# Kernel tuning notes

Measured on AMD Instinct MI355X. Metric: run time of the kernel, lower is better.

The kernel has to match this reference:

```python
import jax, jax.numpy as jnp
import numpy as np

PLANES, RATIO = 512, 4
Q = PLANES // RATIO  # 128
B, H, W = 4, 128, 128


def _dw_stride2(x, k):
    # depthwise 3x3 stride-2 conv, NCHW, kernel [C,1,3,3]
    return jax.lax.conv_general_dilated(
        x, k, window_strides=(2, 2), padding=((1, 1), (1, 1)),
        feature_group_count=x.shape[1],
        dimension_numbers=('NCHW', 'OIHW', 'NCHW'))


def _upsample_bilinear_ac(x, out_h, out_w):
    # bilinear, align_corners=True (matches F.interpolate)
    n, c, h, w = x.shape
    def co(out, ins):
        s = (ins - 1) / (out - 1)
        pos = jnp.arange(out, dtype=jnp.float32) * jnp.float32(s)
        i0 = jnp.floor(pos).astype(jnp.int32)
        i1 = jnp.minimum(i0 + 1, ins - 1)
        return i0, i1, pos - i0.astype(jnp.float32)
    y0, y1, ty = co(out_h, h)
    x0, x1, tx = co(out_w, w)
    rows = x[:, :, y0, :] * (1 - ty)[None, None, :, None] + x[:, :, y1, :] * ty[None, None, :, None]
    return rows[:, :, :, x0] * (1 - tx) + rows[:, :, :, x1] * tx


def setup_inputs() -> dict:
    key = jax.random.key(0)
    ks = jax.random.split(key, 32)
    nrm = lambda k, s, sc=0.05: jax.random.normal(k, s, jnp.float32) * sc
    uni = lambda k, s: jax.random.uniform(k, s, jnp.float32, 0.5, 1.5)
    return {
        'feat': jax.random.normal(ks[0], (B, PLANES, H, W), jnp.float32),
        'w_phi': nrm(ks[1], (2 * Q, PLANES)),
        'bn_phi_s': uni(ks[2], (2 * Q,)), 'bn_phi_b': nrm(ks[3], (2 * Q,)),
        'w_theta': nrm(ks[4], (Q, PLANES)),
        'bn_theta_s': uni(ks[5], (Q,)), 'bn_theta_b': nrm(ks[6], (Q,)),
        'w_adj': nrm(ks[7], (Q, Q)),
        'bn_adj_s': uni(ks[8], (Q,)), 'bn_adj_b': nrm(ks[9], (Q,)),
        'w_wg': nrm(ks[10], (2 * Q, 2 * Q)),
        'bn_wg_s': uni(ks[11], (2 * Q,)), 'bn_wg_b': nrm(ks[12], (2 * Q,)),
        'w_conv3': nrm(ks[13], (PLANES, 2 * Q)),
        'bn3_s': uni(ks[14], (PLANES,)), 'bn3_b': nrm(ks[15], (PLANES,)),
        'w_local1': nrm(ks[16], (PLANES, 1, 3, 3), 0.2),
        'bnl1_s': uni(ks[17], (PLANES,)), 'bnl1_b': nrm(ks[18], (PLANES,)),
        'w_local2': nrm(ks[19], (PLANES, 1, 3, 3), 0.2),
        'bnl2_s': uni(ks[20], (PLANES,)), 'bnl2_b': nrm(ks[21], (PLANES,)),
        'w_local3': nrm(ks[22], (PLANES, 1, 3, 3), 0.2),
        'bnl3_s': uni(ks[23], (PLANES,)), 'bnl3_b': nrm(ks[24], (PLANES,)),
        'gamma': nrm(ks[25], (1,), 0.5),
        'w_final': nrm(ks[26], (PLANES, 2 * PLANES)),
        'bnf_s': uni(ks[27], (PLANES,)), 'bnf_b': nrm(ks[28], (PLANES,)),
    }


def reference(feat, w_phi, bn_phi_s, bn_phi_b, w_theta, bn_theta_s, bn_theta_b,
              w_adj, bn_adj_s, bn_adj_b, w_wg, bn_wg_s, bn_wg_b,
              w_conv3, bn3_s, bn3_b,
              w_local1, bnl1_s, bnl1_b, w_local2, bnl2_s, bnl2_b,
              w_local3, bnl3_s, bnl3_b, gamma, w_final, bnf_s, bnf_b):
    n, c, h, w = feat.shape
    bn2 = lambda x, s, b: x * s[None, :, None, None] + b[None, :, None, None]
    bn1 = lambda x, s, b: x * s[None, :, None] + b[None, :, None]
    conv1x1 = lambda x, wt: jnp.einsum('oc,nchw->nohw', wt, x)

    l = bn2(_dw_stride2(feat, w_local1), bnl1_s, bnl1_b)
    l = bn2(_dw_stride2(l, w_local2), bnl2_s, bnl2_b)
    l = bn2(_dw_stride2(l, w_local3), bnl3_s, bnl3_b)
    nl, cl, hl, wl = l.shape
    v = l.reshape(nl, cl, hl * wl)                      # [n,C,hw]
    energy = jnp.einsum('nck,ndk->ncd', v, v)           # [n,C,C]
    attn = jax.nn.softmax(jnp.max(energy, -1, keepdims=True) - energy, axis=-1)
    cam = jnp.einsum('ncd,ndk->nck', attn, v).reshape(nl, cl, hl, wl)
    l = gamma * cam + l
    local = _upsample_bilinear_ac(l, h, w)
    spatial_local_feat = feat * local + feat

    # ---- graph branch
    q = w_theta.shape[0]
    x_sqz = bn2(conv1x1(feat, w_phi), bn_phi_s, bn_phi_b).reshape(n, 2 * q, h * w)
    b_m = bn2(conv1x1(feat, w_theta), bn_theta_s, bn_theta_b).reshape(n, q, h * w)
    z_idt = jnp.einsum('nck,ndk->ncd', x_sqz, b_m)      # [n,2q,q]
    z = jnp.swapaxes(z_idt, 1, 2)                       # [n,q,2q]
    z = bn1(jnp.einsum('oi,nil->nol', w_adj, z), bn_adj_s, bn_adj_b)
    z = jnp.swapaxes(z, 1, 2) + z_idt                   # [n,2q,q]
    z = bn1(jnp.einsum('oi,nil->nol', w_wg, z), bn_wg_s, bn_wg_b)
    y = jnp.einsum('ncd,ndk->nck', z, b_m).reshape(n, 2 * q, h, w)
    y = bn2(conv1x1(y, w_conv3), bn3_s, bn3_b)
    g_out = jax.nn.relu(feat + y)

    out = bn2(conv1x1(jnp.concatenate([spatial_local_feat, g_out], axis=1), w_final), bnf_s, bnf_b)
    return out
```

## Files before the change

### kernel.cpp

```cpp
#include <hip/hip_runtime.h>
#include <hip/hip_bf16.h>
#include <cstddef>
#include <cstdint>

static constexpr int NB  = 4;
static constexpr int CH  = 512;
static constexpr int HH  = 128;
static constexpr int WWi = 128;
static constexpr int HW  = HH * WWi;
static constexpr int Qd  = 128;
static constexpr int Q2d = 256;

typedef __attribute__((ext_vector_type(8))) short bf8;
typedef __attribute__((ext_vector_type(4))) float f4;

__device__ __forceinline__ short f2bf(float x) {
  __hip_bfloat16 h = __float2bfloat16(x);
  short s; __builtin_memcpy(&s, &h, 2); return s;
}
__device__ __forceinline__ float bfs2f(short u) {
  union { unsigned int i; float f; } x;
  x.i = ((unsigned int)(unsigned short)u) << 16; return x.f;
}

__launch_bounds__(256)
__global__ void dw_conv_bn4(const float* __restrict__ in, float* __restrict__ out,
                            const float* __restrict__ wgt, const float* __restrict__ s,
                            const float* __restrict__ b, int Hi, int Wi, int Ho, int Wo4) {
  int idx = blockIdx.x * 256 + threadIdx.x;
  int q = idx % Wo4; int t = idx / Wo4;
  int ho = t % Ho; t /= Ho;
  int c = t % CH;
  const float* ip = in + (size_t)t * Hi * Wi;
  const float* wp = wgt + c * 9;
  float w[9];
#pragma unroll
  for (int k = 0; k < 9; k++) w[k] = wp[k];
  const int x0 = q * 8;
  float acc0 = 0.f, acc1 = 0.f, acc2 = 0.f, acc3 = 0.f;
#pragma unroll
  for (int kh = 0; kh < 3; kh++) {
    int y = ho * 2 - 1 + kh;
    if ((unsigned)y < (unsigned)Hi) {
      const float* row = ip + (size_t)y * Wi + x0;
      float4 v0 = *(const float4*)row;
      float4 v1 = *(const float4*)(row + 4);
      float left = (x0 > 0) ? row[-1] : 0.f;
      float xs[9] = {left, v0.x, v0.y, v0.z, v0.w, v1.x, v1.y, v1.z, v1.w};
      const float w0 = w[kh * 3 + 0], w1 = w[kh * 3 + 1], w2 = w[kh * 3 + 2];
      acc0 += w0 * xs[0] + w1 * xs[1] + w2 * xs[2];
      acc1 += w0 * xs[2] + w1 * xs[3] + w2 * xs[4];
      acc2 += w0 * xs[4] + w1 * xs[5] + w2 * xs[6];
      acc3 += w0 * xs[6] + w1 * xs[7] + w2 * xs[8];
    }
  }
  const float sc = s[c], bb = b[c];
  float4 o;
  o.x = acc0 * sc + bb; o.y = acc1 * sc + bb;
  o.z = acc2 * sc + bb; o.w = acc3 * sc + bb;
  *(float4*)(out + (size_t)idx * 4) = o;
}

__launch_bounds__(256)
__global__ void lrow_kernel(const float* __restrict__ lcam, float* __restrict__ lrow) {
  int idx = blockIdx.x * 256 + threadIdx.x;
  int wcol = idx & 127; int t = idx >> 7;
  int hy = t & 15; t >>= 4;
  float pos = wcol * (15.f / 127.f);
  int x0 = (int)pos; if (x0 > 15) x0 = 15;
  float tx = pos - x0;
  int x1 = x0 + 1; if (x1 > 15) x1 = 15;
  const float* lc = lcam + ((size_t)t * 16 + hy) * 16;
  lrow[idx] = lc[x0] * (1.f - tx) + lc[x1] * tx;
}

__launch_bounds__(256)
__global__ void cvt_f32_bf16(const float* __restrict__ in, short* __restrict__ out, int n4) {
  int i = blockIdx.x * 256 + threadIdx.x;
  if (i >= n4) return;
  float4 v = ((const float4*)in)[i];
  short tmp[4] = {f2bf(v.x), f2bf(v.y), f2bf(v.z), f2bf(v.w)};
  short4 o; __builtin_memcpy(&o, tmp, 8);
  ((short4*)out)[i] = o;
}

__device__ __forceinline__ int sls(int row, int slot) {
  return row * 64 + ((slot ^ (((row >> 1) ^ (row >> 3)) & 7)) << 3);
}

__device__ __forceinline__ void stg64_dma(const short* __restrict__ src, size_t stride,
                                          int kb, short* lds, int t) {
  const int lane = t & 63, w = t >> 6;
#pragma unroll
  for (int i2 = 0; i2 < 4; i2++) {
    int r0 = w * 32 + i2 * 8;
    int row = r0 + (lane >> 3);
    int sl = (lane & 7) ^ (((row >> 1) ^ (row >> 3)) & 7);
    const short* g = src + (size_t)row * stride + kb + sl * 8;
    short* l = lds + r0 * 64;
    __builtin_amdgcn_global_load_lds(
        (const __attribute__((address_space(1))) unsigned int*)g,
        (__attribute__((address_space(3))) unsigned int*)l, 16, 0, 0);
  }
}

__device__ __forceinline__ void stg64_b16(const short* __restrict__ src, size_t stride,
                                          int kb, short* lds, int t) {
#pragma unroll
  for (int i = 0; i < 4; i++) {
    int chunk = t + i * 256;
    int row = chunk >> 3, slot = chunk & 7;
    bf8 v = *(const bf8*)(src + (size_t)row * stride + kb + slot * 8);
    *(bf8*)(lds + sls(row, slot)) = v;
  }
}
__device__ __forceinline__ void stg64_f32(const float* __restrict__ src, size_t stride,
                                          int kb, short* lds, int t) {
#pragma unroll
  for (int i = 0; i < 4; i++) {
    int chunk = t + i * 256;
    int row = chunk >> 3, slot = chunk & 7;
    const float* sp = src + (size_t)row * stride + kb + slot * 8;
    float4 v0 = *(const float4*)sp, v1 = *(const float4*)(sp + 4);
    union { short s[8]; bf8 v; } u;
    u.s[0] = f2bf(v0.x); u.s[1] = f2bf(v0.y); u.s[2] = f2bf(v0.z); u.s[3] = f2bf(v0.w);
    u.s[4] = f2bf(v1.x); u.s[5] = f2bf(v1.y); u.s[6] = f2bf(v1.z); u.s[7] = f2bf(v1.w);
    *(bf8*)(lds + sls(row, slot)) = u.v;
  }
}
__device__ __forceinline__ void stg64_t32(const float* __restrict__ src, size_t sstride,
                                          int pb, short* lds, int t) {
#pragma unroll
  for (int i2 = 0; i2 < 4; i2++) {
    int chunk = t + i2 * 256;
    int c = (chunk >> 3) & 63;
    int p8 = ((chunk & 7) | ((chunk >> 6) & 8)) * 8;
    const float* fr = src + (size_t)c * sstride + pb + p8;
    float4 f0 = *(const float4*)fr, f1 = *(const float4*)(fr + 4);
    float fv[8];
    __builtin_memcpy(&fv[0], &f0, 16); __builtin_memcpy(&fv[4], &f1, 16);
    int slot = c >> 3, eidx = c & 7;
#pragma unroll
    for (int e = 0; e < 8; e++) {
      lds[sls(p8 + e, slot) + eidx] = f2bf(fv[e]);
    }
  }
}
__device__ __forceinline__ void stg64_t16(const short* __restrict__ src, size_t sstride,
                                          int pb, short* lds, int t) {
#pragma unroll
  for (int i2 = 0; i2 < 4; i2++) {
    int chunk = t + i2 * 256;
    int c = (chunk >> 3) & 63;
    int p8 = ((chunk & 7) | ((chunk >> 6) & 8)) * 8;
    bf8 v = *(const bf8*)(src + (size_t)c * sstride + pb + p8);
    int slot = c >> 3, eidx = c & 7;
#pragma unroll
    for (int e = 0; e < 8; e++) {
      lds[sls(p8 + e, slot) + eidx] = v[e];
    }
  }
}
__device__ __forceinline__ bf8 fragld64(const short* lds, int row, int kk, int lg) {
  return *(const bf8*)(lds + sls(row, kk * 4 + lg));
}

__launch_bounds__(256)
__global__ void slf_build_T(const float* __restrict__ feat, const float* __restrict__ lrw,
                            short* __restrict__ slfbT, int h0) {
  const int cb = blockIdx.x * 64;
  const int hh = blockIdx.y;
  const int n  = blockIdx.z;
  const int h  = hh + h0;
  const int t  = threadIdx.x;
  __shared__ __align__(16) short lT[8192];
  const float posy = h * (15.f / 127.f);
  int hy0 = (int)posy; if (hy0 > 15) hy0 = 15;
  int hy1 = hy0 + 1; if (hy1 > 15) hy1 = 15;
  const float tyv = posy - hy0;
#pragma unroll
  for (int i2 = 0; i2 < 4; i2++) {
    int chunk = t + i2 * 256;
    int c = (chunk >> 3) & 63;
    int w8 = ((chunk & 7) | ((chunk >> 6) & 8)) * 8;
    size_t cidx = (size_t)(n * CH) + cb + c;
    const float* fr = feat + cidx * HW + h * WWi + w8;
    const float* l0r = lrw + (cidx * 16 + hy0) * WWi + w8;
    const float* l1r = lrw + (cidx * 16 + hy1) * WWi + w8;
    float4 f0 = *(const float4*)fr, f1 = *(const float4*)(fr + 4);
    float4 a0 = *(const float4*)l0r, a1 = *(const float4*)(l0r + 4);
    float4 b0 = *(const float4*)l1r, b1 = *(const float4*)(l1r + 4);
    float fv[8], av[8], bv[8];
    __builtin_memcpy(&fv[0], &f0, 16); __builtin_memcpy(&fv[4], &f1, 16);
    __builtin_memcpy(&av[0], &a0, 16); __builtin_memcpy(&av[4], &a1, 16);
    __builtin_memcpy(&bv[0], &b0, 16); __builtin_memcpy(&bv[4], &b1, 16);
    int slot = c >> 3, eidx = c & 7;
#pragma unroll
    for (int e = 0; e < 8; e++) {
      float v = fv[e] * (1.f + av[e] + (bv[e] - av[e]) * tyv);
      lT[sls(w8 + e, slot) + eidx] = f2bf(v);
    }
  }
  __syncthreads();
#pragma unroll
  for (int i2 = 0; i2 < 4; i2++) {
    int chunk = t + i2 * 256;
    int w = chunk >> 3, slot = chunk & 7;
    bf8 v = *(const bf8*)(lT + sls(w, slot));
    *(bf8*)(slfbT + (((size_t)(n * 64) + hh) * WWi + w) * CH + cb + slot * 8) = v;
  }
}

__launch_bounds__(256)
__global__ void energy_mfma(const float* __restrict__ l3, float* __restrict__ energy) {
  const int c0 = blockIdx.x * 128;
  const int d0 = blockIdx.y * 128;
  const int n = blockIdx.z;
  const int t = threadIdx.x;
  const int lane16 = t & 15, lg = (t >> 4) & 3, wave = t >> 6;
  const int wm = (wave >> 1) * 64, wn = (wave & 1) * 64;
  __shared__ __align__(16) short lA[8192], lB[8192];
  const float* srcA = l3 + ((size_t)n * CH + c0) * 256;
  const float* srcB = l3 + ((size_t)n * CH + d0) * 256;
  f4 acc[4][4];
#pragma unroll
  for (int i = 0; i < 4; i++)
#pragma unroll
    for (int j = 0; j < 4; j++) acc[i][j] = (f4)0.f;
  for (int kb = 0; kb < 256; kb += 64) {
    stg64_f32(srcA, 256, kb, lA, t);
    stg64_f32(srcB, 256, kb, lB, t);
    __syncthreads();
#pragma unroll
    for (int kk = 0; kk < 2; kk++) {
      bf8 av[4], bv[4];
#pragma unroll
      for (int i = 0; i < 4; i++) av[i] = fragld64(lA, wm + i * 16 + lane16, kk, lg);
#pragma unroll
      for (int j = 0; j < 4; j++) bv[j] = fragld64(lB, wn + j * 16 + lane16, kk, lg);
#pragma unroll
      for (int i = 0; i < 4; i++)
#pragma unroll
        for (int j = 0; j < 4; j++)
          acc[i][j] = __builtin_amdgcn_mfma_f32_16x16x32_bf16(av[i], bv[j], acc[i][j], 0, 0, 0);
    }
    __syncthreads();
  }
#pragma unroll
  for (int i = 0; i < 4; i++)
#pragma unroll
    for (int j = 0; j < 4; j++) {
      int d = d0 + wn + j * 16 + lane16;
#pragma unroll
      for (int r = 0; r < 4; r++) {
        int c = c0 + wm + i * 16 + lg * 4 + r;
        energy[((size_t)n * CH + c) * CH + d] = acc[i][j][r];
      }
    }
}

__launch_bounds__(256)
__global__ void softmax_attn(float* __restrict__ energy) {
  float* row = energy + (size_t)blockIdx.x * CH;
  int t = threadIdx.x;
  __shared__ float red[256];
  float e0 = row[t], e1 = row[t + 256];
  red[t] = fminf(e0, e1);
  __syncthreads();
  for (int s = 128; s > 0; s >>= 1) {
    if (t < s) red[t] = fminf(red[t], red[t + s]);
    __syncthreads();
  }
  float emin = red[0];
  __syncthreads();
  float w0 = __expf(emin - e0), w1 = __expf(emin - e1);
  red[t] = w0 + w1;
  __syncthreads();
  for (int s = 128; s > 0; s >>= 1) {
    if (t < s) red[t] += red[t + s];
    __syncthreads();
  }
  float inv = 1.f / red[0];
  row[t] = w0 * inv;
  row[t + 256] = w1 * inv;
}

__launch_bounds__(256)
__global__ void cam_mfma(const float* __restrict__ attn, const float* __restrict__ l3,
                         const float* __restrict__ gamma, float* __restrict__ lcam) {
  const int pb = blockIdx.x * 128;
  const int mb = blockIdx.y * 128;
  const int n = blockIdx.z;
  const int t = threadIdx.x;
  const int lane16 = t & 15, lg = (t >> 4) & 3, wave = t >> 6;
  const int wm = (wave >> 1) * 64, wn = (wave & 1) * 64;
  __shared__ __align__(16) short lA[8192], lB[8192];
  const float* srcA = attn + ((size_t)n * CH + mb) * CH;
  const float gm = gamma[0];
  f4 acc[4][4];
#pragma unroll
  for (int i = 0; i < 4; i++)
#pragma unroll
    for (int j = 0; j < 4; j++) acc[i][j] = (f4)0.f;
  for (int kb = 0; kb < 512; kb += 64) {
    stg64_f32(srcA, CH, kb, lA, t);
    stg64_t32(l3 + ((size_t)n * CH + kb) * 256, 256, pb, lB, t);
    __syncthreads();
#pragma unroll
    for (int kk = 0; kk < 2; kk++) {
      bf8 av[4], bv[4];
#pragma unroll
      for (int i = 0; i < 4; i++) av[i] = fragld64(lA, wm + i * 16 + lane16, kk, lg);
#pragma unroll
      for (int j = 0; j < 4; j++) bv[j] = fragld64(lB, wn + j * 16 + lane16, kk, lg);
#pragma unroll
      for (int i = 0; i < 4; i++)
#pragma unroll
        for (int j = 0; j < 4; j++)
          acc[i][j] = __builtin_amdgcn_mfma_f32_16x16x32_bf16(av[i], bv[j], acc[i][j], 0, 0, 0);
    }
    __syncthreads();
  }
#pragma unroll
  for (int i = 0; i < 4; i++)
#pragma unroll
    for (int j = 0; j < 4; j++) {
      int p = pb + wn + j * 16 + lane16;
#pragma unroll
      for (int r = 0; r < 4; r++) {
        int c = mb + wm + i * 16 + lg * 4 + r;
        size_t idx = ((size_t)n * CH + c) * 256 + p;
        lcam[idx] = gm * acc[i][j][r] + l3[idx];
      }
    }
}

__launch_bounds__(256)
__global__ void theta_mfma2(const short* __restrict__ wthb, const float* __restrict__ feat,
                            const float* __restrict__ s, const float* __restrict__ b,
                            short* __restrict__ bmb) {
  const int pb = blockIdx.x * 128;
  const int n = blockIdx.y;
  const int t = threadIdx.x;
  const int lane16 = t & 15, lg = (t >> 4) & 3, wave = t >> 6;
  const int wm = (wave >> 1) * 64, wn = (wave & 1) * 64;
  __shared__ __align__(16) short lA[8192], lB[8192];
  f4 acc[4][4];
#pragma unroll
  for (int i = 0; i < 4; i++)
#pragma unroll
    for (int j = 0; j < 4; j++) acc[i][j] = (f4)0.f;
  for (int kb = 0; kb < 512; kb += 64) {
    stg64_dma(wthb, 512, kb, lA, t);
    stg64_t32(feat + ((size_t)(n * CH) + kb) * HW, HW, pb, lB, t);
    __syncthreads();
#pragma unroll
    for (int kk = 0; kk < 2; kk++) {
      bf8 av[4], bv[4];
#pragma unroll
      for (int i = 0; i < 4; i++) av[i] = fragld64(lA, wm + i * 16 + lane16, kk, lg);
#pragma unroll
      for (int j = 0; j < 4; j++) bv[j] = fragld64(lB, wn + j * 16 + lane16, kk, lg);
#pragma unroll
      for (int i = 0; i < 4; i++)
#pragma unroll
        for (int j = 0; j < 4; j++)
          acc[i][j] = __builtin_amdgcn_mfma_f32_16x16x32_bf16(av[i], bv[j], acc[i][j], 0, 0, 0);
    }
    __syncthreads();
  }
#pragma unroll
  for (int i = 0; i < 4; i++)
#pragma unroll
    for (int j = 0; j < 4; j++) {
      int p = pb + wn + j * 16 + lane16;
#pragma unroll
      for (int r = 0; r < 4; r++) {
        int d = wm + i * 16 + lg * 4 + r;
        bmb[((size_t)(n * Qd) + d) * HW + p] = f2bf(s[d] * acc[i][j][r] + b[d]);
      }
    }
}

__launch_bounds__(256)
__global__ void rowsum_bf(const short* __restrict__ bmb, float* __restrict__ rs) {
  int row = blockIdx.x;
  int t = threadIdx.x;
  const short* r = bmb + (size_t)row * HW;
  float a = 0.f;
  for (int p = t * 8; p < HW; p += 2048) {
    bf8 v = *(const bf8*)(r + p);
#pragma unroll
    for (int e = 0; e < 8; e++) a += bfs2f(v[e]);
  }
  __shared__ float red[256];
  red[t] = a;
  __syncthreads();
  for (int s = 128; s > 0; s >>= 1) {
    if (t < s) red[t] += red[t + s];
    __syncthreads();
  }
  if (t == 0) rs[row] = red[0];
}

__launch_bounds__(256)
__global__ void m1_mfma2(const float* __restrict__ feat, const short* __restrict__ bmb,
                         float* __restrict__ m1p) {
  const int c0 = blockIdx.x * 128;
  const int kc = blockIdx.y;
  const int n = blockIdx.z;
  const int t = threadIdx.x;
  const int lane16 = t & 15, lg = (t >> 4) & 3, wave = t >> 6;
  const int wm = (wave >> 1) * 64, wn = (wave & 1) * 64;
  __shared__ __align__(16) short lA[8192], lB[8192];
  const float* srcA = feat + ((size_t)(n * CH) + c0) * HW;
  const short* srcB = bmb + (size_t)(n * Qd) * HW;
  f4 acc[4][4];
#pragma unroll
  for (int i = 0; i < 4; i++)
#pragma unroll
    for (int j = 0; j < 4; j++) acc[i][j] = (f4)0.f;
  const int kend = kc * 512 + 512;
  for (int kb = kc * 512; kb < kend; kb += 64) {
    stg64_f32(srcA, HW, kb, lA, t);
    stg64_dma(srcB, HW, kb, lB, t);
    __syncthreads();
#pragma unroll
    for (int kk = 0; kk < 2; kk++) {
      bf8 av[4], bv[4];
#pragma unroll
      for (int i = 0; i < 4; i++) av[i] = fragld64(lA, wm + i * 16 + lane16, kk, lg);
#pragma unroll
      for (int j = 0; j < 4; j++) bv[j] = fragld64(lB, wn + j * 16 + lane16, kk, lg);
#pragma unroll
      for (int i = 0; i < 4; i++)
#pragma unroll
        for (int j = 0; j < 4; j++)
          acc[i][j] = __builtin_amdgcn_mfma_f32_16x16x32_bf16(av[i], bv[j], acc[i][j], 0, 0, 0);
    }
    __syncthreads();
  }
#pragma unroll
  for (int i = 0; i < 4; i++)
#pragma unroll
    for (int j = 0; j < 4; j++) {
      int d = wn + j * 16 + lane16;
#pragma unroll
      for (int r = 0; r < 4; r++) {
        int c = c0 + wm + i * 16 + lg * 4 + r;
        m1p[(((size_t)kc * NB + n) * CH + c) * Qd + d] = acc[i][j][r];
      }
    }
}

__launch_bounds__(256)
__global__ void m1_reduce(const float* __restrict__ m1p, float* __restrict__ m1) {
  int idx = blockIdx.x * 256 + threadIdx.x;
  float a = 0.f;
#pragma unroll
  for (int kc = 0; kc < 32; kc++) a += m1p[(size_t)kc * (NB * CH * Qd) + idx];
  m1[idx] = a;
}

__launch_bounds__(128)
__global__ void zidt_kernel(const float* __restrict__ m1, const float* __restrict__ wphi,
                            const float* __restrict__ sp, const float* __restrict__ bp,
                            const float* __restrict__ rs, float* __restrict__ zidt) {
  int n = blockIdx.y, c = blockIdx.x, d = threadIdx.x;
  __shared__ float wrow[512];
  for (int i = d; i < 512; i += 128) wrow[i] = wphi[(size_t)c * 512 + i];
  __syncthreads();
  const float* mb = m1 + (size_t)n * CH * Qd;
  float acc = 0.f;
#pragma unroll 4
  for (int i = 0; i < 512; i++) acc += wrow[i] * mb[i * Qd + d];
  zidt[((size_t)n * Q2d + c) * Qd + d] = sp[c] * acc + bp[c] * rs[n * Qd + d];
}

__launch_bounds__(128)
__global__ void z3_kernel(const float* __restrict__ zidt, const float* __restrict__ wadj,
                          const float* __restrict__ sa, const float* __restrict__ ba,
                          float* __restrict__ z3) {
  int n = blockIdx.y, c = blockIdx.x, d = threadIdx.x;
  __shared__ float zr[128];
  zr[d] = zidt[((size_t)n * Q2d + c) * Qd + d];
  __syncthreads();
  const float* wrow = wadj + (size_t)d * 128;
  float acc = 0.f;
#pragma unroll 4
  for (int i = 0; i < 128; i++) acc += wrow[i] * zr[i];
  z3[((size_t)n * Q2d + c) * Qd + d] = sa[d] * acc + ba[d] + zr[d];
}

__launch_bounds__(128)
__global__ void z4_kernel(const float* __restrict__ z3, const float* __restrict__ wwg,
                          const float* __restrict__ sw, const float* __restrict__ bw,
                          float* __restrict__ z4) {
  int n = blockIdx.y, o = blockIdx.x, d = threadIdx.x;
  __shared__ float wrow[256];
  wrow[d] = wwg[(size_t)o * 256 + d];
  wrow[d + 128] = wwg[(size_t)o * 256 + 128 + d];
  __syncthreads();
  const float* zb = z3 + (size_t)n * Q2d * Qd;
  float acc = 0.f;
#pragma unroll 4
  for (int i = 0; i < 256; i++) acc += wrow[i] * zb[i * Qd + d];
  z4[((size_t)n * Q2d + o) * Qd + d] = sw[o] * acc + bw[o];
}

__launch_bounds__(128)
__global__ void wz_kernel(const float* __restrict__ z4, const float* __restrict__ wc3,
                          const float* __restrict__ s3, float* __restrict__ wz) {
  int n = blockIdx.y, o = blockIdx.x, d = threadIdx.x;
  __shared__ float wrow[256];
  wrow[d] = wc3[(size_t)o * 256 + d];
  wrow[d + 128] = wc3[(size_t)o * 256 + 128 + d];
  __syncthreads();
  const float* zb = z4 + (size_t)n * Q2d * Qd;
  float acc = 0.f;
#pragma unroll 4
  for (int i = 0; i < 256; i++) acc += wrow[i] * zb[i * Qd + d];
  wz[((size_t)n * CH + o) * Qd + d] = s3[o] * acc;
}

__launch_bounds__(256)
__global__ void ygout_mfma2(const float* __restrict__ wz, const short* __restrict__ bmb,
                            const float* __restrict__ feat, const float* __restrict__ b3,
                            short* __restrict__ goutT) {
  const int pb = blockIdx.x * 128;
  const int mb = blockIdx.y * 128;
  const int n = blockIdx.z;
  const int t = threadIdx.x;
  const int lane16 = t & 15, lg = (t >> 4) & 3, wave = t >> 6;
  const int wm = (wave >> 1) * 64, wn = (wave & 1) * 64;
  __shared__ __align__(16) short lA[8192], lB[8192];
  const float* srcA = wz + ((size_t)(n * CH) + mb) * Qd;
  f4 acc[4][4];
#pragma unroll
  for (int i = 0; i < 4; i++)
#pragma unroll
    for (int j = 0; j < 4; j++) acc[i][j] = (f4)0.f;
  for (int kb = 0; kb < 128; kb += 64) {
    stg64_f32(srcA, Qd, kb, lA, t);
    stg64_t16(bmb + ((size_t)(n * Qd) + kb) * HW, HW, pb, lB, t);
    __syncthreads();
#pragma unroll
    for (int kk = 0; kk < 2; kk++) {
      bf8 av[4], bv[4];
#pragma unroll
      for (int i = 0; i < 4; i++) av[i] = fragld64(lA, wm + i * 16 + lane16, kk, lg);
#pragma unroll
      for (int j = 0; j < 4; j++) bv[j] = fragld64(lB, wn + j * 16 + lane16, kk, lg);
#pragma unroll
      for (int i = 0; i < 4; i++)
#pragma unroll
        for (int j = 0; j < 4; j++)
          acc[i][j] = __builtin_amdgcn_mfma_f32_16x16x32_bf16(av[i], bv[j], acc[i][j], 0, 0, 0);
    }
    __syncthreads();
  }
#pragma unroll
  for (int i = 0; i < 4; i++)
#pragma unroll
    for (int j = 0; j < 4; j++) {
      int p = pb + wn + j * 16 + lane16;
      int c0 = mb + wm + i * 16 + lg * 4;
      union { short s[4]; short4 v; } u;
#pragma unroll
      for (int r = 0; r < 4; r++) {
        float g = feat[((size_t)(n * CH) + c0 + r) * HW + p] + acc[i][j][r] + b3[c0 + r];
        u.s[r] = f2bf(g > 0.f ? g : 0.f);
      }
      *(short4*)(goutT + ((size_t)(n * HW) + p) * CH + c0) = u.v;
    }
}

__launch_bounds__(256)
__global__ void final_mfma(const short* __restrict__ wfb, const short* __restrict__ slfbT,
                           const int h0, const short* __restrict__ goutT,
                           const float* __restrict__ fs, const float* __restrict__ fb,
                           float* __restrict__ out) {
  const int h = blockIdx.x + h0;
  const int pb = h * WWi;
  const int mb = blockIdx.y * 128;
  const int n = blockIdx.z;
  const int t = threadIdx.x;
  const int lane16 = t & 15, lg = (t >> 4) & 3, wave = t >> 6;
  const int wm = (wave >> 1) * 64, wn = (wave & 1) * 64;
  __shared__ __align__(16) short lA[8192], lB[8192];
  const short* slfRows = slfbT + ((size_t)(n * 64) + (h - h0)) * WWi * CH;
  const short* goutRows = goutT + ((size_t)(n * HW) + pb) * CH;
  f4 acc[4][4];
#pragma unroll
  for (int i = 0; i < 4; i++)
#pragma unroll
    for (int j = 0; j < 4; j++) acc[i][j] = (f4)0.f;

  for (int kb = 0; kb < 1024; kb += 64) {
    stg64_dma(wfb + (size_t)mb * 1024, 1024, kb, lA, t);
    if (kb < 512) {
      stg64_dma(slfRows, CH, kb, lB, t);
    } else {
      stg64_dma(goutRows, CH, kb - 512, lB, t);
    }
    __syncthreads();
#pragma unroll
    for (int kk = 0; kk < 2; kk++) {
      bf8 avf[4], bvf[4];
#pragma unroll
      for (int i = 0; i < 4; i++) avf[i] = fragld64(lA, wm + i * 16 + lane16, kk, lg);
#pragma unroll
      for (int j = 0; j < 4; j++) bvf[j] = fragld64(lB, wn + j * 16 + lane16, kk, lg);
#pragma unroll
      for (int i = 0; i < 4; i++)
#pragma unroll
        for (int j = 0; j < 4; j++)
          acc[i][j] = __builtin_amdgcn_mfma_f32_16x16x32_bf16(avf[i], bvf[j], acc[i][j], 0, 0, 0);
    }
    __syncthreads();
  }
#pragma unroll
  for (int i = 0; i < 4; i++)
#pragma unroll
    for (int j = 0; j < 4; j++) {
      int p = pb + wn + j * 16 + lane16;
#pragma unroll
      for (int r = 0; r < 4; r++) {
        int m = mb + wm + i * 16 + lg * 4 + r;
        out[((size_t)(n * CH) + m) * HW + p] = fs[m] * acc[i][j][r] + fb[m];
      }
    }
}

extern "C" void kernel_launch(void* const* d_in, const int* in_sizes, int n_in,
                              void* d_out, int out_size, void* d_ws, size_t ws_size,
                              hipStream_t stream) {
  (void)in_sizes; (void)n_in; (void)out_size; (void)ws_size;
  const float* feat      = (const float*)d_in[0];
  const float* w_phi     = (const float*)d_in[1];
  const float* bn_phi_s  = (const float*)d_in[2];
  const float* bn_phi_b  = (const float*)d_in[3];
  const float* w_theta   = (const float*)d_in[4];
  const float* bn_theta_s= (const float*)d_in[5];
  const float* bn_theta_b= (const float*)d_in[6];
  const float* w_adj     = (const float*)d_in[7];
  const float* bn_adj_s  = (const float*)d_in[8];
  const float* bn_adj_b  = (const float*)d_in[9];
  const float* w_wg      = (const float*)d_in[10];
  const float* bn_wg_s   = (const float*)d_in[11];
  const float* bn_wg_b   = (const float*)d_in[12];
  const float* w_conv3   = (const float*)d_in[13];
  const float* bn3_s     = (const float*)d_in[14];
  const float* bn3_b     = (const float*)d_in[15];
  const float* w_l1      = (const float*)d_in[16];
  const float* bnl1_s    = (const float*)d_in[17];
  const float* bnl1_b    = (const float*)d_in[18];
  const float* w_l2      = (const float*)d_in[19];
  const float* bnl2_s    = (const float*)d_in[20];
  const float* bnl2_b    = (const float*)d_in[21];
  const float* w_l3      = (const float*)d_in[22];
  const float* bnl3_s    = (const float*)d_in[23];
  const float* bnl3_b    = (const float*)d_in[24];
  const float* gamma     = (const float*)d_in[25];
  const float* w_final   = (const float*)d_in[26];
  const float* bnf_s     = (const float*)d_in[27];
  const float* bnf_b     = (const float*)d_in[28];

  float* out = (float*)d_out;
  float* l1 = out;
  float* l2 = l1 + (size_t)8388608;
  float* l3 = l2 + (size_t)2097152;
  short* wthb = (short*)(l3 + (size_t)524288);

  float* ws   = (float*)d_ws;
  float* lcam = ws;
  float* lrw  = lcam + (size_t)4 * 512 * 256;
  float* bm_region = lrw + (size_t)4 * 512 * 16 * 128;
  short* bmb  = (short*)bm_region;
  float* rsum = bm_region + (size_t)4 * 128 * 16384;
  float* M1   = rsum + 512;
  float* M1p_old = M1 + (size_t)4 * 512 * 128;
  float* zidt = M1p_old + (size_t)8 * 4 * 512 * 128;
  float* z3b  = zidt + (size_t)4 * 256 * 128;
  float* z4b  = z3b + (size_t)4 * 256 * 128;
  float* wzb  = z4b + (size_t)4 * 256 * 128;
  short* gout = (short*)(wzb + (size_t)4 * 512 * 128);
  short* wfb  = (short*)M1p_old;
  float* m1p  = (float*)gout;
  float* energy = (float*)M1p_old;
  short* slfb = (short*)bm_region;

  dw_conv_bn4<<<dim3(4 * 512 * 64 * 16 / 256), 256, 0, stream>>>(feat, l1, w_l1, bnl1_s, bnl1_b, 128, 128, 64, 16);
  dw_conv_bn4<<<dim3(4 * 512 * 32 * 8 / 256), 256, 0, stream>>>(l1, l2, w_l2, bnl2_s, bnl2_b, 64, 64, 32, 8);
  dw_conv_bn4<<<dim3(4 * 512 * 16 * 4 / 256), 256, 0, stream>>>(l2, l3, w_l3, bnl3_s, bnl3_b, 32, 32, 16, 4);
  energy_mfma<<<dim3(4, 4, 4), 256, 0, stream>>>(l3, energy);
  softmax_attn<<<dim3(4 * 512), 256, 0, stream>>>(energy);
  cam_mfma<<<dim3(2, 4, 4), 256, 0, stream>>>(energy, l3, gamma, lcam);
  lrow_kernel<<<dim3(4 * 512 * 16 * 128 / 256), 256, 0, stream>>>(lcam, lrw);

  cvt_f32_bf16<<<dim3(64), 256, 0, stream>>>(w_theta, wthb, 16384);
  theta_mfma2<<<dim3(128, 4), 256, 0, stream>>>(wthb, feat, bn_theta_s, bn_theta_b, bmb);
  rowsum_bf<<<dim3(512), 256, 0, stream>>>(bmb, rsum);
  m1_mfma2<<<dim3(4, 32, 4), 256, 0, stream>>>(feat, bmb, m1p);
  m1_reduce<<<dim3(1024), 256, 0, stream>>>(m1p, M1);
  zidt_kernel<<<dim3(256, 4), 128, 0, stream>>>(M1, w_phi, bn_phi_s, bn_phi_b, rsum, zidt);
  z3_kernel<<<dim3(256, 4), 128, 0, stream>>>(zidt, w_adj, bn_adj_s, bn_adj_b, z3b);
  z4_kernel<<<dim3(256, 4), 128, 0, stream>>>(z3b, w_wg, bn_wg_s, bn_wg_b, z4b);
  wz_kernel<<<dim3(512, 4), 128, 0, stream>>>(z4b, w_conv3, bn3_s, wzb);
  ygout_mfma2<<<dim3(128, 4, 4), 256, 0, stream>>>(wzb, bmb, feat, bn3_b, gout);

  cvt_f32_bf16<<<dim3(512), 256, 0, stream>>>(w_final, wfb, 131072);

  slf_build_T<<<dim3(8, 64, 4), 256, 0, stream>>>(feat, lrw, slfb, 0);
  final_mfma<<<dim3(64, 4, 4), 256, 0, stream>>>(wfb, slfb, 0, gout, bnf_s, bnf_b, out);
  slf_build_T<<<dim3(8, 64, 4), 256, 0, stream>>>(feat, lrw, slfb, 64);
  final_mfma<<<dim3(64, 4, 4), 256, 0, stream>>>(wfb, slfb, 64, gout, bnf_s, bnf_b, out);
}
```

Before: 458.1 us.

## Pre-convert feat to bf16, emit transposed bm, fuse zidt into z3

Adds an up-front kernel that converts the full feat tensor to bf16 so that theta_mfma2 and m1_mfma2 read half the bytes and can use the direct bf16 staging path. theta_mfma2 now also writes a transposed bf16 copy of b_m, which lets ygout_mfma2 stage its B operand with a contiguous load instead of a transposing one. zidt and z3 are merged into one kernel, dropping a launch and an intermediate round trip. The cost is an extra full pass over feat (read 128MB fp32, write 64MB bf16) plus an extra write of b_m. featb is placed in scratch space inside the output buffer at a fixed offset, which risks overlapping live data there.

Measured after the change: 497.2 us. 8.5% more time.

```diff
diff --git a/kernel.cpp b/kernel.cpp
--- a/kernel.cpp
+++ b/kernel.cpp
@@ -336,9 +336,9 @@
 }
 
 __launch_bounds__(256)
-__global__ void theta_mfma2(const short* __restrict__ wthb, const float* __restrict__ feat,
+__global__ void theta_mfma2(const short* __restrict__ wthb, const short* __restrict__ featb,
                             const float* __restrict__ s, const float* __restrict__ b,
-                            short* __restrict__ bmb) {
+                            short* __restrict__ bmb, short* __restrict__ bmbT) {
   const int pb = blockIdx.x * 128;
   const int n = blockIdx.y;
   const int t = threadIdx.x;
@@ -352,7 +352,7 @@
     for (int j = 0; j < 4; j++) acc[i][j] = (f4)0.f;
   for (int kb = 0; kb < 512; kb += 64) {
     stg64_dma(wthb, 512, kb, lA, t);
-    stg64_t32(feat + ((size_t)(n * CH) + kb) * HW, HW, pb, lB, t);
+    stg64_t16(featb + ((size_t)(n * CH) + kb) * HW, HW, pb, lB, t);
     __syncthreads();
 #pragma unroll
     for (int kk = 0; kk < 2; kk++) {
@@ -374,11 +374,15 @@
 #pragma unroll
     for (int j = 0; j < 4; j++) {
       int p = pb + wn + j * 16 + lane16;
+      int d0 = wm + i * 16 + lg * 4;
+      union { short s[4]; short4 v; } u;
 #pragma unroll
       for (int r = 0; r < 4; r++) {
-        int d = wm + i * 16 + lg * 4 + r;
-        bmb[((size_t)(n * Qd) + d) * HW + p] = f2bf(s[d] * acc[i][j][r] + b[d]);
+        short bv = f2bf(s[d0 + r] * acc[i][j][r] + b[d0 + r]);
+        u.s[r] = bv;
+        bmb[((size_t)(n * Qd) + d0 + r) * HW + p] = bv;
       }
+      *(short4*)(bmbT + ((size_t)(n * HW) + p) * Qd + d0) = u.v;
     }
 }
 
@@ -404,7 +408,7 @@
 }
 
 __launch_bounds__(256)
-__global__ void m1_mfma2(const float* __restrict__ feat, const short* __restrict__ bmb,
+__global__ void m1_mfma2(const short* __restrict__ featb, const short* __restrict__ bmb,
                          float* __restrict__ m1p) {
   const int c0 = blockIdx.x * 128;
   const int kc = blockIdx.y;
@@ -413,7 +417,7 @@
   const int lane16 = t & 15, lg = (t >> 4) & 3, wave = t >> 6;
   const int wm = (wave >> 1) * 64, wn = (wave & 1) * 64;
   __shared__ __align__(16) short lA[8192], lB[8192];
-  const float* srcA = feat + ((size_t)(n * CH) + c0) * HW;
+  const short* srcA = featb + ((size_t)(n * CH) + c0) * HW;
   const short* srcB = bmb + (size_t)(n * Qd) * HW;
   f4 acc[4][4];
 #pragma unroll
@@ -422,7 +426,7 @@
     for (int j = 0; j < 4; j++) acc[i][j] = (f4)0.f;
   const int kend = kc * 512 + 512;
   for (int kb = kc * 512; kb < kend; kb += 64) {
-    stg64_f32(srcA, HW, kb, lA, t);
+    stg64_dma(srcA, HW, kb, lA, t);
     stg64_dma(srcB, HW, kb, lB, t);
     __syncthreads();
 #pragma unroll
@@ -463,33 +467,27 @@
 }
 
 __launch_bounds__(128)
-__global__ void zidt_kernel(const float* __restrict__ m1, const float* __restrict__ wphi,
-                            const float* __restrict__ sp, const float* __restrict__ bp,
-                            const float* __restrict__ rs, float* __restrict__ zidt) {
+__global__ void z3_fused(const float* __restrict__ m1, const float* __restrict__ wphi,
+                         const float* __restrict__ sp, const float* __restrict__ bp,
+                         const float* __restrict__ rs, const float* __restrict__ wadj,
+                         const float* __restrict__ sa, const float* __restrict__ ba,
+                         float* __restrict__ z3) {
   int n = blockIdx.y, c = blockIdx.x, d = threadIdx.x;
   __shared__ float wrow[512];
+  __shared__ float zr[128];
   for (int i = d; i < 512; i += 128) wrow[i] = wphi[(size_t)c * 512 + i];
   __syncthreads();
   const float* mb = m1 + (size_t)n * CH * Qd;
   float acc = 0.f;
 #pragma unroll 4
   for (int i = 0; i < 512; i++) acc += wrow[i] * mb[i * Qd + d];
-  zidt[((size_t)n * Q2d + c) * Qd + d] = sp[c] * acc + bp[c] * rs[n * Qd + d];
-}
-
-__launch_bounds__(128)
-__global__ void z3_kernel(const float* __restrict__ zidt, const float* __restrict__ wadj,
-                          const float* __restrict__ sa, const float* __restrict__ ba,
-                          float* __restrict__ z3) {
-  int n = blockIdx.y, c = blockIdx.x, d = threadIdx.x;
-  __shared__ float zr[128];
-  zr[d] = zidt[((size_t)n * Q2d + c) * Qd + d];
-  __syncthreads();
-  const float* wrow = wadj + (size_t)d * 128;
-  float acc = 0.f;
+  zr[d] = sp[c] * acc + bp[c] * rs[n * Qd + d];
+  __syncthreads();
+  const float* wr = wadj + (size_t)d * 128;
+  float acc2 = 0.f;
 #pragma unroll 4
-  for (int i = 0; i < 128; i++) acc += wrow[i] * zr[i];
-  z3[((size_t)n * Q2d + c) * Qd + d] = sa[d] * acc + ba[d] + zr[d];
+  for (int i = 0; i < 128; i++) acc2 += wr[i] * zr[i];
+  z3[((size_t)n * Q2d + c) * Qd + d] = sa[d] * acc2 + ba[d] + zr[d];
 }
 
 __launch_bounds__(128)
@@ -524,7 +522,7 @@
 }
 
 __launch_bounds__(256)
-__global__ void ygout_mfma2(const float* __restrict__ wz, const short* __restrict__ bmb,
+__global__ void ygout_mfma2(const float* __restrict__ wz, const short* __restrict__ bmbT,
                             const float* __restrict__ feat, const float* __restrict__ b3,
                             short* __restrict__ goutT) {
   const int pb = blockIdx.x * 128;
@@ -535,6 +533,7 @@
   const int wm = (wave >> 1) * 64, wn = (wave & 1) * 64;
   __shared__ __align__(16) short lA[8192], lB[8192];
   const float* srcA = wz + ((size_t)(n * CH) + mb) * Qd;
+  const short* srcB = bmbT + ((size_t)(n * HW) + pb) * Qd;
   f4 acc[4][4];
 #pragma unroll
   for (int i = 0; i < 4; i++)
@@ -542,7 +541,7 @@
     for (int j = 0; j < 4; j++) acc[i][j] = (f4)0.f;
   for (int kb = 0; kb < 128; kb += 64) {
     stg64_f32(srcA, Qd, kb, lA, t);
-    stg64_t16(bmb + ((size_t)(n * Qd) + kb) * HW, HW, pb, lB, t);
+    stg64_dma(srcB, Qd, kb, lB, t);
     __syncthreads();
 #pragma unroll
     for (int kk = 0; kk < 2; kk++) {
@@ -671,12 +670,14 @@
   float* l2 = l1 + (size_t)8388608;
   float* l3 = l2 + (size_t)2097152;
   short* wthb = (short*)(l3 + (size_t)524288);
+  short* featb = (short*)(out + (size_t)12000000);
 
   float* ws   = (float*)d_ws;
   float* lcam = ws;
   float* lrw  = lcam + (size_t)4 * 512 * 256;
   float* bm_region = lrw + (size_t)4 * 512 * 16 * 128;
   short* bmb  = (short*)bm_region;
+  short* bmbT = (short*)(bm_region + (size_t)4194304);
   float* rsum = bm_region + (size_t)4 * 128 * 16384;
   float* M1   = rsum + 512;
   float* M1p_old = M1 + (size_t)4 * 512 * 128;
@@ -690,6 +691,8 @@
   float* energy = (float*)M1p_old;
   short* slfb = (short*)bm_region;
 
+  cvt_f32_bf16<<<dim3(32768), 256, 0, stream>>>(feat, featb, 8388608);
+
   dw_conv_bn4<<<dim3(4 * 512 * 64 * 16 / 256), 256, 0, stream>>>(feat, l1, w_l1, bnl1_s, bnl1_b, 128, 128, 64, 16);
   dw_conv_bn4<<<dim3(4 * 512 * 32 * 8 / 256), 256, 0, stream>>>(l1, l2, w_l2, bnl2_s, bnl2_b, 64, 64, 32, 8);
   dw_conv_bn4<<<dim3(4 * 512 * 16 * 4 / 256), 256, 0, stream>>>(l2, l3, w_l3, bnl3_s, bnl3_b, 32, 32, 16, 4);
@@ -699,15 +702,14 @@
   lrow_kernel<<<dim3(4 * 512 * 16 * 128 / 256), 256, 0, stream>>>(lcam, lrw);
 
   cvt_f32_bf16<<<dim3(64), 256, 0, stream>>>(w_theta, wthb, 16384);
-  theta_mfma2<<<dim3(128, 4), 256, 0, stream>>>(wthb, feat, bn_theta_s, bn_theta_b, bmb);
+  theta_mfma2<<<dim3(128, 4), 256, 0, stream>>>(wthb, featb, bn_theta_s, bn_theta_b, bmb, bmbT);
   rowsum_bf<<<dim3(512), 256, 0, stream>>>(bmb, rsum);
-  m1_mfma2<<<dim3(4, 32, 4), 256, 0, stream>>>(feat, bmb, m1p);
+  m1_mfma2<<<dim3(4, 32, 4), 256, 0, stream>>>(featb, bmb, m1p);
   m1_reduce<<<dim3(1024), 256, 0, stream>>>(m1p, M1);
-  zidt_kernel<<<dim3(256, 4), 128, 0, stream>>>(M1, w_phi, bn_phi_s, bn_phi_b, rsum, zidt);
-  z3_kernel<<<dim3(256, 4), 128, 0, stream>>>(zidt, w_adj, bn_adj_s, bn_adj_b, z3b);
+  z3_fused<<<dim3(256, 4), 128, 0, stream>>>(M1, w_phi, bn_phi_s, bn_phi_b, rsum, w_adj, bn_adj_s, bn_adj_b, z3b);
   z4_kernel<<<dim3(256, 4), 128, 0, stream>>>(z3b, w_wg, bn_wg_s, bn_wg_b, z4b);
   wz_kernel<<<dim3(512, 4), 128, 0, stream>>>(z4b, w_conv3, bn3_s, wzb);
-  ygout_mfma2<<<dim3(128, 4, 4), 256, 0, stream>>>(wzb, bmb, feat, bn3_b, gout);
+  ygout_mfma2<<<dim3(128, 4, 4), 256, 0, stream>>>(wzb, bmbT, feat, bn3_b, gout);
 
   cvt_f32_bf16<<<dim3(512), 256, 0, stream>>>(w_final, wfb, 131072);
 
```
